# Kernel tuning notes

Hardware: AMD Instinct MI355X
Metric: run time of the kernel (lower is better)

Reference implementation:

```python
import jax, jax.numpy as jnp
from jax import lax
import numpy as np

B, T, D, H, OUT = 128, 1024, 256, 256, 2


def _rnn_layer(inp, W_xh, W_hh, b):
    # inp: [B, T, Din]; returns [B, T, H]
    h0 = jnp.zeros((inp.shape[0], W_hh.shape[0]), inp.dtype)

    def step(h, x_t):
        h_new = jnp.tanh(x_t @ W_xh.T + h @ W_hh.T + b)
        return h_new, h_new

    _, ys = lax.scan(step, h0, jnp.swapaxes(inp, 0, 1))  # ys: [T, B, H]
    return jnp.swapaxes(ys, 0, 1)


def setup_inputs() -> dict:
    key = jax.random.key(0)
    ks = jax.random.split(key, 8)
    s_in = 1.0 / np.sqrt(H)  # torch nn.RNN init scale
    x = jax.random.normal(ks[0], (B, T, D), dtype=jnp.float32)
    W_xh0 = jax.random.uniform(ks[1], (H, D), jnp.float32, -s_in, s_in)
    W_hh0 = jax.random.uniform(ks[2], (H, H), jnp.float32, -s_in, s_in)
    b0 = jax.random.uniform(ks[3], (H,), jnp.float32, -s_in, s_in)
    W_xh1 = jax.random.uniform(ks[4], (H, H), jnp.float32, -s_in, s_in)
    W_hh1 = jax.random.uniform(ks[5], (H, H), jnp.float32, -s_in, s_in)
    b1 = jax.random.uniform(ks[6], (H,), jnp.float32, -s_in, s_in)
    fc_w = jax.random.uniform(ks[7], (OUT, H), jnp.float32, -s_in, s_in)
    fc_b = jnp.zeros((OUT,), jnp.float32)
    return {"x": x, "W_xh0": W_xh0, "W_hh0": W_hh0, "b0": b0,
            "W_xh1": W_xh1, "W_hh1": W_hh1, "b1": b1,
            "fc_w": fc_w, "fc_b": fc_b}


def reference(x, W_xh0, W_hh0, b0, W_xh1, W_hh1, b1, fc_w, fc_b):
    h1 = _rnn_layer(x, W_xh0, W_hh0, b0)   # [B, T, H]
    h2 = _rnn_layer(h1, W_xh1, W_hh1, b1)  # [B, T, H]
    # linear head on last timestep
    return h2[:, -1, :] @ fc_w.T + fc_b    # [B, OUT]
```

## Files before the change

### kernel.cpp

```cpp
#include <hip/hip_runtime.h>

#define Bsz 128
#define Tn  1024
#define Dn  256
#define Hn  256

typedef _Float16 f16;
typedef _Float16 f16x4 __attribute__((ext_vector_type(4)));
typedef _Float16 f16x8 __attribute__((ext_vector_type(8)));
typedef float f32x4 __attribute__((ext_vector_type(4)));

__device__ __forceinline__ float tanh_fast(float x) {
    float e = __builtin_amdgcn_exp2f(x * 2.88539008177793f);
    return 1.0f - 2.0f * __builtin_amdgcn_rcpf(e + 1.0f);
}

__device__ __forceinline__ void wg_barrier() {
    asm volatile("s_waitcnt lgkmcnt(0)\n\ts_barrier" ::: "memory");
}


__global__ __launch_bounds__(256, 2) void k_xproj(
    const float* __restrict__ x, const float* __restrict__ W,
    const float* __restrict__ bias, float* __restrict__ preT)
{
    __shared__ __align__(16) f16 xt[128][264];
    const int tid = threadIdx.x;
    const int t = blockIdx.x;

    for (int i = tid; i < 128 * 64; i += 256) {
        int row = i >> 6, c4 = i & 63;
        float4 v = *(const float4*)(x + ((size_t)row * Tn + t) * Dn + c4 * 4);
        f16x4 tv = { (f16)v.x, (f16)v.y, (f16)v.z, (f16)v.w };
        *(f16x4*)(&xt[row][c4 * 4]) = tv;
    }

    const int lane = tid & 63, l15 = lane & 15, quad = lane >> 4;
    const int w = tid >> 6;

    f16x8 wf[4][8];
    #pragma unroll
    for (int jn = 0; jn < 4; jn++) {
        int j = w * 64 + jn * 16 + l15;
        #pragma unroll
        for (int kk = 0; kk < 8; kk++)
            #pragma unroll
            for (int e = 0; e < 8; e++)
                wf[jn][kk][e] = (f16)W[(size_t)j * Dn + kk * 32 + quad * 8 + e];
    }
    float4 bi[4];
    #pragma unroll
    for (int jn = 0; jn < 4; jn++)
        bi[jn] = *(const float4*)(bias + w * 64 + jn * 16 + quad * 4);

    __syncthreads();

    #pragma unroll 1
    for (int bblk = 0; bblk < 8; bblk++) {
        f32x4 acc[4];
        #pragma unroll
        for (int jn = 0; jn < 4; jn++)
            acc[jn] = (f32x4){bi[jn].x, bi[jn].y, bi[jn].z, bi[jn].w};
        #pragma unroll
        for (int kk = 0; kk < 8; kk++) {
            f16x8 xb = *(const f16x8*)(&xt[bblk * 16 + l15][kk * 32 + quad * 8]);
            #pragma unroll
            for (int jn = 0; jn < 4; jn++)
                acc[jn] = __builtin_amdgcn_mfma_f32_16x16x32_f16(wf[jn][kk], xb, acc[jn], 0, 0, 0);
        }
        #pragma unroll
        for (int jn = 0; jn < 4; jn++) {
            int j0 = w * 64 + jn * 16 + quad * 4;
            *(f32x4*)(preT + ((size_t)t * Bsz + bblk * 16 + l15) * Hn + j0) = acc[jn];
        }
    }
}

__global__ __launch_bounds__(512, 1) void k_fused(
    const float* __restrict__ Whh0, const float* __restrict__ Wxh1,
    const float* __restrict__ Whh1, const float* __restrict__ b1v,
    const float* __restrict__ fcw,  const float* __restrict__ fcb,
    const float* __restrict__ preT, float* __restrict__ out)
{
    __shared__ __align__(16) f16 h1f[2][4096];
    __shared__ __align__(16) f16 h2f[2][4096];

    const int tid  = threadIdx.x;
    const int lane = tid & 63, l15 = lane & 15, quad = lane >> 4;
    const int w    = tid >> 6;
    const int colbase = w * 32;
    const int bg   = blockIdx.x * 16;

    for (int i = tid; i < 4096; i += 512) {
        h1f[0][i] = (f16)0.0f; h1f[1][i] = (f16)0.0f;
        h2f[0][i] = (f16)0.0f; h2f[1][i] = (f16)0.0f;
    }

    f16x8 wh0[2][8], wx[2][8], wh1[2][8];
    #pragma unroll
    for (int jn = 0; jn < 2; jn++) {
        int j = colbase + jn * 16 + l15;
        #pragma unroll
        for (int kk = 0; kk < 8; kk++)
            #pragma unroll
            for (int e = 0; e < 8; e++) {
                int o = (int)((size_t)j * Hn + kk * 32 + quad * 8 + e);
                wh0[jn][kk][e] = (f16)Whh0[o];
                wx [jn][kk][e] = (f16)Wxh1[o];
                wh1[jn][kk][e] = (f16)Whh1[o];
            }
    }
    float4 bi[2];
    #pragma unroll
    for (int jn = 0; jn < 2; jn++)
        bi[jn] = *(const float4*)(b1v + colbase + jn * 16 + quad * 4);

    int wroff[2];
    #pragma unroll
    for (int jn = 0; jn < 2; jn++) {
        int n0 = colbase + jn * 16 + quad * 4;
        wroff[jn] = (n0 >> 5) * 512 + ((n0 >> 3) & 3) * 128 + l15 * 8 + (n0 & 7);
    }

    const float* pp = preT + ((size_t)(bg + l15)) * Hn + colbase + quad * 4;

    f32x4 pnv[2];
    pnv[0] = *(const f32x4*)(pp);
    pnv[1] = *(const f32x4*)(pp + 16);
    __syncthreads();

#define FSTEP_FULL(PR, I, TF) { \
    f32x4 accA[2]; \
    accA[0] = pnv[0]; accA[1] = pnv[1]; \
    pnv[0] = *(const f32x4*)(pp + (size_t)(TF) * (Bsz * Hn)); \
    pnv[1] = *(const f32x4*)(pp + (size_t)(TF) * (Bsz * Hn) + 16); \
    f16x8 hb1[8]; \
    _Pragma("unroll") for (int kk = 0; kk < 8; kk++) { \
        hb1[kk] = *(const f16x8*)(&h1f[(PR)^1][kk * 512 + lane * 8]); \
        accA[0] = __builtin_amdgcn_mfma_f32_16x16x32_f16(wh0[0][kk], hb1[kk], accA[0], 0, 0, 0); \
        accA[1] = __builtin_amdgcn_mfma_f32_16x16x32_f16(wh0[1][kk], hb1[kk], accA[1], 0, 0, 0); \
    } \
     \
    _Pragma("unroll") for (int jn = 0; jn < 2; jn++) { \
        f16x4 t1v = { (f16)tanh_fast(accA[jn][0]), (f16)tanh_fast(accA[jn][1]), \
                      (f16)tanh_fast(accA[jn][2]), (f16)tanh_fast(accA[jn][3]) }; \
        *(f16x4*)(&h1f[(PR)][wroff[jn]]) = t1v; \
    } \
    f32x4 accB[2]; \
    _Pragma("unroll") for (int jn = 0; jn < 2; jn++) \
        accB[jn] = (f32x4){bi[jn].x, bi[jn].y, bi[jn].z, bi[jn].w}; \
    _Pragma("unroll") for (int kk = 0; kk < 8; kk++) { \
        f16x8 hb2 = *(const f16x8*)(&h2f[(PR)][kk * 512 + lane * 8]); \
        accB[0] = __builtin_amdgcn_mfma_f32_16x16x32_f16(wx [0][kk], hb1[kk], accB[0], 0, 0, 0); \
        accB[1] = __builtin_amdgcn_mfma_f32_16x16x32_f16(wx [1][kk], hb1[kk], accB[1], 0, 0, 0); \
        accB[0] = __builtin_amdgcn_mfma_f32_16x16x32_f16(wh1[0][kk], hb2, accB[0], 0, 0, 0); \
        accB[1] = __builtin_amdgcn_mfma_f32_16x16x32_f16(wh1[1][kk], hb2, accB[1], 0, 0, 0); \
    } \
    _Pragma("unroll") for (int jn = 0; jn < 2; jn++) { \
        f16x4 t2v = { (f16)tanh_fast(accB[jn][0]), (f16)tanh_fast(accB[jn][1]), \
                      (f16)tanh_fast(accB[jn][2]), (f16)tanh_fast(accB[jn][3]) }; \
        *(f16x4*)(&h2f[(PR)^1][wroff[jn]]) = t2v; \
    } \
    wg_barrier(); \
}

    {
        f32x4 accA[2];
        accA[0] = pnv[0]; accA[1] = pnv[1];
        pnv[0] = *(const f32x4*)(pp + (size_t)1 * (Bsz * Hn));
        pnv[1] = *(const f32x4*)(pp + (size_t)1 * (Bsz * Hn) + 16);
        #pragma unroll
        for (int kk = 0; kk < 8; kk++) {
            f16x8 hb1 = *(const f16x8*)(&h1f[1][kk * 512 + lane * 8]);
            accA[0] = __builtin_amdgcn_mfma_f32_16x16x32_f16(wh0[0][kk], hb1, accA[0], 0, 0, 0);
            accA[1] = __builtin_amdgcn_mfma_f32_16x16x32_f16(wh0[1][kk], hb1, accA[1], 0, 0, 0);
        }
        #pragma unroll
        for (int jn = 0; jn < 2; jn++) {
            f16x4 t1v = { (f16)tanh_fast(accA[jn][0]), (f16)tanh_fast(accA[jn][1]),
                          (f16)tanh_fast(accA[jn][2]), (f16)tanh_fast(accA[jn][3]) };
            *(f16x4*)(&h1f[0][wroff[jn]]) = t1v;
        }
        wg_barrier();
    }

    #pragma unroll 1
    for (int tp = 0; tp < 511; ++tp) {
        const int t1 = 2 * tp + 1;
        FSTEP_FULL(1, t1, (t1 + 1))
        FSTEP_FULL(0, (t1 + 1), (t1 + 2))
    }
    FSTEP_FULL(1, 1023, 1023)
#undef FSTEP_FULL

    {
        f32x4 accB[2];
        #pragma unroll
        for (int jn = 0; jn < 2; jn++)
            accB[jn] = (f32x4){bi[jn].x, bi[jn].y, bi[jn].z, bi[jn].w};
        #pragma unroll
        for (int kk = 0; kk < 8; kk++) {
            f16x8 hb1 = *(const f16x8*)(&h1f[1][kk * 512 + lane * 8]);
            f16x8 hb2 = *(const f16x8*)(&h2f[0][kk * 512 + lane * 8]);
            accB[0] = __builtin_amdgcn_mfma_f32_16x16x32_f16(wx [0][kk], hb1, accB[0], 0, 0, 0);
            accB[1] = __builtin_amdgcn_mfma_f32_16x16x32_f16(wx [1][kk], hb1, accB[1], 0, 0, 0);
            accB[0] = __builtin_amdgcn_mfma_f32_16x16x32_f16(wh1[0][kk], hb2, accB[0], 0, 0, 0);
            accB[1] = __builtin_amdgcn_mfma_f32_16x16x32_f16(wh1[1][kk], hb2, accB[1], 0, 0, 0);
        }
        #pragma unroll
        for (int jn = 0; jn < 2; jn++) {
            f16x4 t2v = { (f16)tanh_fast(accB[jn][0]), (f16)tanh_fast(accB[jn][1]),
                          (f16)tanh_fast(accB[jn][2]), (f16)tanh_fast(accB[jn][3]) };
            *(f16x4*)(&h2f[1][wroff[jn]]) = t2v;
        }
        wg_barrier();
    }

    if (tid < 256) {
        const int bl = tid >> 4, o = (tid >> 3) & 1, kc = tid & 7;
        float s = 0.f;
        #pragma unroll
        for (int kq = 0; kq < 32; kq++) {
            int k = kc * 32 + kq;
            f16 hv = h2f[1][(k >> 5) * 512 + ((k >> 3) & 3) * 128 + bl * 8 + (k & 7)];
            s += (float)hv * fcw[o * Hn + k];
        }
        s += __shfl_down(s, 4);
        s += __shfl_down(s, 2);
        s += __shfl_down(s, 1);
        if (kc == 0)
            out[(bg + bl) * 2 + o] = s + fcb[o];
    }
}

extern "C" void kernel_launch(void* const* d_in, const int* in_sizes, int n_in,
                              void* d_out, int out_size, void* d_ws, size_t ws_size,
                              hipStream_t stream) {
    const float* x    = (const float*)d_in[0];
    const float* Wxh0 = (const float*)d_in[1];
    const float* Whh0 = (const float*)d_in[2];
    const float* b0   = (const float*)d_in[3];
    const float* Wxh1 = (const float*)d_in[4];
    const float* Whh1 = (const float*)d_in[5];
    const float* b1   = (const float*)d_in[6];
    const float* fcw  = (const float*)d_in[7];
    const float* fcb  = (const float*)d_in[8];
    float* out = (float*)d_out;

    float* preT = (float*)d_ws;

    k_xproj<<<dim3(Tn),       dim3(256), 0, stream>>>(x, Wxh0, b0, preT);
    k_fused<<<dim3(Bsz / 16), dim3(512), 0, stream>>>(Whh0, Wxh1, Whh1, b1,
                                                      fcw, fcb, preT, out);
}
```

Baseline: 1.372 ms.

## Split RNN layers into producer/consumer workgroups pipelined via global memory flags

Layer 0 and layer 1 now run on separate workgroups: 8 producer blocks compute layer-0 hidden states and publish each timestep to a global buffer with a release flag, while 8 consumer blocks spin on the flag and compute layer 1, prefetching the next h1 step from global memory. The goal is to take layer-0 work off layer 1's serial critical path, so each step's dependent chain is shorter and the two layers overlap. In exchange, every step pays global-memory stores and loads plus flag polling latency. The scheme also depends on both producer and consumer blocks being resident at the same time, and the flag is reset to zero at the end so later calls start clean.

```diff
diff --git a/kernel.cpp b/kernel.cpp
--- a/kernel.cpp
+++ b/kernel.cpp
@@ -9,6 +9,11 @@
 typedef _Float16 f16x4 __attribute__((ext_vector_type(4)));
 typedef _Float16 f16x8 __attribute__((ext_vector_type(8)));
 typedef float f32x4 __attribute__((ext_vector_type(4)));
+
+#define MF(A, B, C) __builtin_amdgcn_mfma_f32_16x16x32_f16((A), (B), (C), 0, 0, 0)
+
+__device__ unsigned long long g_h1[8ull * 1024 * 1024];
+__device__ int g_flag[8 * 64];
 
 __device__ __forceinline__ float tanh_fast(float x) {
     float e = __builtin_amdgcn_exp2f(x * 2.88539008177793f);
@@ -66,7 +71,7 @@
             f16x8 xb = *(const f16x8*)(&xt[bblk * 16 + l15][kk * 32 + quad * 8]);
             #pragma unroll
             for (int jn = 0; jn < 4; jn++)
-                acc[jn] = __builtin_amdgcn_mfma_f32_16x16x32_f16(wf[jn][kk], xb, acc[jn], 0, 0, 0);
+                acc[jn] = MF(wf[jn][kk], xb, acc[jn]);
         }
         #pragma unroll
         for (int jn = 0; jn < 4; jn++) {
@@ -82,38 +87,16 @@
     const float* __restrict__ fcw,  const float* __restrict__ fcb,
     const float* __restrict__ preT, float* __restrict__ out)
 {
-    __shared__ __align__(16) f16 h1f[2][4096];
-    __shared__ __align__(16) f16 h2f[2][4096];
+    __shared__ __align__(16) f16 hbuf[2][4096];
 
     const int tid  = threadIdx.x;
     const int lane = tid & 63, l15 = lane & 15, quad = lane >> 4;
     const int w    = tid >> 6;
     const int colbase = w * 32;
-    const int bg   = blockIdx.x * 16;
-
-    for (int i = tid; i < 4096; i += 512) {
-        h1f[0][i] = (f16)0.0f; h1f[1][i] = (f16)0.0f;
-        h2f[0][i] = (f16)0.0f; h2f[1][i] = (f16)0.0f;
-    }
-
-    f16x8 wh0[2][8], wx[2][8], wh1[2][8];
-    #pragma unroll
-    for (int jn = 0; jn < 2; jn++) {
-        int j = colbase + jn * 16 + l15;
-        #pragma unroll
-        for (int kk = 0; kk < 8; kk++)
-            #pragma unroll
-            for (int e = 0; e < 8; e++) {
-                int o = (int)((size_t)j * Hn + kk * 32 + quad * 8 + e);
-                wh0[jn][kk][e] = (f16)Whh0[o];
-                wx [jn][kk][e] = (f16)Wxh1[o];
-                wh1[jn][kk][e] = (f16)Whh1[o];
-            }
-    }
-    float4 bi[2];
-    #pragma unroll
-    for (int jn = 0; jn < 2; jn++)
-        bi[jn] = *(const float4*)(b1v + colbase + jn * 16 + quad * 4);
+    const int gidx = blockIdx.x & 7;
+    const int bg   = gidx * 16;
+
+    for (int i = tid; i < 8192; i += 512) ((f16*)hbuf)[i] = (f16)0.0f;
 
     int wroff[2];
     #pragma unroll
@@ -122,114 +105,177 @@
         wroff[jn] = (n0 >> 5) * 512 + ((n0 >> 3) & 3) * 128 + l15 * 8 + (n0 & 7);
     }
 
-    const float* pp = preT + ((size_t)(bg + l15)) * Hn + colbase + quad * 4;
-
-    f32x4 pnv[2];
-    pnv[0] = *(const f32x4*)(pp);
-    pnv[1] = *(const f32x4*)(pp + 16);
-    __syncthreads();
-
-#define FSTEP_FULL(PR, I, TF) { \
+    unsigned long long* hg = g_h1 + (size_t)gidx * (1024 * 1024);
+    int* flagp = &g_flag[gidx * 64];
+
+    if (blockIdx.x < 8) {
+        f16x8 wh0[2][8];
+        #pragma unroll
+        for (int jn = 0; jn < 2; jn++) {
+            int j = colbase + jn * 16 + l15;
+            #pragma unroll
+            for (int kk = 0; kk < 8; kk++)
+                #pragma unroll
+                for (int e = 0; e < 8; e++)
+                    wh0[jn][kk][e] = (f16)Whh0[(size_t)j * Hn + kk * 32 + quad * 8 + e];
+        }
+        const float* pp = preT + ((size_t)(bg + l15)) * Hn + colbase + quad * 4;
+        f32x4 pnv0 = *(const f32x4*)(pp);
+        f32x4 pnv1 = *(const f32x4*)(pp + 16);
+        __syncthreads();
+
+#define PSTEP(P, I, TF) { \
     f32x4 accA[2]; \
-    accA[0] = pnv[0]; accA[1] = pnv[1]; \
-    pnv[0] = *(const f32x4*)(pp + (size_t)(TF) * (Bsz * Hn)); \
-    pnv[1] = *(const f32x4*)(pp + (size_t)(TF) * (Bsz * Hn) + 16); \
-    f16x8 hb1[8]; \
+    accA[0] = pnv0; accA[1] = pnv1; \
+    pnv0 = *(const f32x4*)(pp + (size_t)(TF) * (Bsz * Hn)); \
+    pnv1 = *(const f32x4*)(pp + (size_t)(TF) * (Bsz * Hn) + 16); \
     _Pragma("unroll") for (int kk = 0; kk < 8; kk++) { \
-        hb1[kk] = *(const f16x8*)(&h1f[(PR)^1][kk * 512 + lane * 8]); \
-        accA[0] = __builtin_amdgcn_mfma_f32_16x16x32_f16(wh0[0][kk], hb1[kk], accA[0], 0, 0, 0); \
-        accA[1] = __builtin_amdgcn_mfma_f32_16x16x32_f16(wh0[1][kk], hb1[kk], accA[1], 0, 0, 0); \
-    } \
-     \
+        f16x8 hb = *(const f16x8*)(&hbuf[(P)^1][kk * 512 + lane * 8]); \
+        accA[0] = MF(wh0[0][kk], hb, accA[0]); \
+        accA[1] = MF(wh0[1][kk], hb, accA[1]); \
+    } \
     _Pragma("unroll") for (int jn = 0; jn < 2; jn++) { \
-        f16x4 t1v = { (f16)tanh_fast(accA[jn][0]), (f16)tanh_fast(accA[jn][1]), \
-                      (f16)tanh_fast(accA[jn][2]), (f16)tanh_fast(accA[jn][3]) }; \
-        *(f16x4*)(&h1f[(PR)][wroff[jn]]) = t1v; \
-    } \
+        union { f16x4 v; unsigned long long u; } t1; \
+        t1.v = (f16x4){ (f16)tanh_fast(accA[jn][0]), (f16)tanh_fast(accA[jn][1]), \
+                        (f16)tanh_fast(accA[jn][2]), (f16)tanh_fast(accA[jn][3]) }; \
+        *(f16x4*)(&hbuf[(P)][wroff[jn]]) = t1.v; \
+        __hip_atomic_store(hg + (size_t)(I) * 1024 + (wroff[jn] >> 2), t1.u, \
+                           __ATOMIC_RELAXED, __HIP_MEMORY_SCOPE_AGENT); \
+    } \
+    asm volatile("s_waitcnt vmcnt(0) lgkmcnt(0)\n\ts_barrier" ::: "memory"); \
+    if (tid == 0) \
+        __hip_atomic_store(flagp, (I) + 1, __ATOMIC_RELEASE, __HIP_MEMORY_SCOPE_AGENT); \
+}
+
+        #pragma unroll 1
+        for (int tp = 0; tp < 511; ++tp) {
+            const int t0 = 2 * tp;
+            PSTEP(0, t0, (t0 + 1))
+            PSTEP(1, (t0 + 1), (t0 + 2))
+        }
+        PSTEP(0, 1022, 1023)
+        PSTEP(1, 1023, 1023)
+#undef PSTEP
+    } else {
+        f16x8 wx[2][8], wh1[2][8];
+        #pragma unroll
+        for (int jn = 0; jn < 2; jn++) {
+            int j = colbase + jn * 16 + l15;
+            #pragma unroll
+            for (int kk = 0; kk < 8; kk++)
+                #pragma unroll
+                for (int e = 0; e < 8; e++) {
+                    int o = (int)((size_t)j * Hn + kk * 32 + quad * 8 + e);
+                    wx [jn][kk][e] = (f16)Wxh1[o];
+                    wh1[jn][kk][e] = (f16)Whh1[o];
+                }
+        }
+        float4 bi[2];
+        #pragma unroll
+        for (int jn = 0; jn < 2; jn++)
+            bi[jn] = *(const float4*)(b1v + colbase + jn * 16 + quad * 4);
+        __syncthreads();
+
+        int fval = __hip_atomic_load(flagp, __ATOMIC_RELAXED, __HIP_MEMORY_SCOPE_AGENT);
+        while (fval < 1) {
+            __builtin_amdgcn_s_sleep(2);
+            fval = __hip_atomic_load(flagp, __ATOMIC_RELAXED, __HIP_MEMORY_SCOPE_AGENT);
+        }
+        __builtin_amdgcn_fence(__ATOMIC_ACQUIRE, "agent");
+        f16x8 bufA[8], bufB[8];
+        {
+            unsigned long long* hp = hg + lane * 2;
+            #pragma unroll
+            for (int kk = 0; kk < 8; kk++) {
+                union { unsigned long long u[2]; f16x8 v; } tb;
+                tb.u[0] = __hip_atomic_load(hp + kk * 128,     __ATOMIC_RELAXED, __HIP_MEMORY_SCOPE_AGENT);
+                tb.u[1] = __hip_atomic_load(hp + kk * 128 + 1, __ATOMIC_RELAXED, __HIP_MEMORY_SCOPE_AGENT);
+                bufA[kk] = tb.v;
+            }
+        }
+        fval = __hip_atomic_load(flagp, __ATOMIC_RELAXED, __HIP_MEMORY_SCOPE_AGENT);
+
+#define CSTEP(P, I, CURB, NXTB) { \
+    int fchk = fval; \
+    fval = __hip_atomic_load(flagp, __ATOMIC_RELAXED, __HIP_MEMORY_SCOPE_AGENT); \
+    if (fchk < (I) + 2) { \
+        do { __builtin_amdgcn_s_sleep(2); \
+             fchk = __hip_atomic_load(flagp, __ATOMIC_RELAXED, __HIP_MEMORY_SCOPE_AGENT); \
+        } while (fchk < (I) + 2); \
+        fval = fchk; \
+    } \
+    __builtin_amdgcn_fence(__ATOMIC_ACQUIRE, "agent"); \
+    { unsigned long long* hp = hg + (size_t)((I) + 1) * 1024 + lane * 2; \
+      _Pragma("unroll") for (int kk = 0; kk < 8; kk++) { \
+        union { unsigned long long u[2]; f16x8 v; } tb; \
+        tb.u[0] = __hip_atomic_load(hp + kk * 128,     __ATOMIC_RELAXED, __HIP_MEMORY_SCOPE_AGENT); \
+        tb.u[1] = __hip_atomic_load(hp + kk * 128 + 1, __ATOMIC_RELAXED, __HIP_MEMORY_SCOPE_AGENT); \
+        NXTB[kk] = tb.v; } } \
     f32x4 accB[2]; \
-    _Pragma("unroll") for (int jn = 0; jn < 2; jn++) \
-        accB[jn] = (f32x4){bi[jn].x, bi[jn].y, bi[jn].z, bi[jn].w}; \
+    accB[0] = (f32x4){bi[0].x, bi[0].y, bi[0].z, bi[0].w}; \
+    accB[1] = (f32x4){bi[1].x, bi[1].y, bi[1].z, bi[1].w}; \
     _Pragma("unroll") for (int kk = 0; kk < 8; kk++) { \
-        f16x8 hb2 = *(const f16x8*)(&h2f[(PR)][kk * 512 + lane * 8]); \
-        accB[0] = __builtin_amdgcn_mfma_f32_16x16x32_f16(wx [0][kk], hb1[kk], accB[0], 0, 0, 0); \
-        accB[1] = __builtin_amdgcn_mfma_f32_16x16x32_f16(wx [1][kk], hb1[kk], accB[1], 0, 0, 0); \
-        accB[0] = __builtin_amdgcn_mfma_f32_16x16x32_f16(wh1[0][kk], hb2, accB[0], 0, 0, 0); \
-        accB[1] = __builtin_amdgcn_mfma_f32_16x16x32_f16(wh1[1][kk], hb2, accB[1], 0, 0, 0); \
+        f16x8 hb2 = *(const f16x8*)(&hbuf[(P)][kk * 512 + lane * 8]); \
+        accB[0] = MF(wx [0][kk], CURB[kk], accB[0]); \
+        accB[1] = MF(wx [1][kk], CURB[kk], accB[1]); \
+        accB[0] = MF(wh1[0][kk], hb2, accB[0]); \
+        accB[1] = MF(wh1[1][kk], hb2, accB[1]); \
     } \
     _Pragma("unroll") for (int jn = 0; jn < 2; jn++) { \
         f16x4 t2v = { (f16)tanh_fast(accB[jn][0]), (f16)tanh_fast(accB[jn][1]), \
                       (f16)tanh_fast(accB[jn][2]), (f16)tanh_fast(accB[jn][3]) }; \
-        *(f16x4*)(&h2f[(PR)^1][wroff[jn]]) = t2v; \
+        *(f16x4*)(&hbuf[(P)^1][wroff[jn]]) = t2v; \
     } \
     wg_barrier(); \
 }
-
-    {
-        f32x4 accA[2];
-        accA[0] = pnv[0]; accA[1] = pnv[1];
-        pnv[0] = *(const f32x4*)(pp + (size_t)1 * (Bsz * Hn));
-        pnv[1] = *(const f32x4*)(pp + (size_t)1 * (Bsz * Hn) + 16);
-        #pragma unroll
-        for (int kk = 0; kk < 8; kk++) {
-            f16x8 hb1 = *(const f16x8*)(&h1f[1][kk * 512 + lane * 8]);
-            accA[0] = __builtin_amdgcn_mfma_f32_16x16x32_f16(wh0[0][kk], hb1, accA[0], 0, 0, 0);
-            accA[1] = __builtin_amdgcn_mfma_f32_16x16x32_f16(wh0[1][kk], hb1, accA[1], 0, 0, 0);
-        }
-        #pragma unroll
-        for (int jn = 0; jn < 2; jn++) {
-            f16x4 t1v = { (f16)tanh_fast(accA[jn][0]), (f16)tanh_fast(accA[jn][1]),
-                          (f16)tanh_fast(accA[jn][2]), (f16)tanh_fast(accA[jn][3]) };
-            *(f16x4*)(&h1f[0][wroff[jn]]) = t1v;
-        }
-        wg_barrier();
-    }
-
-    #pragma unroll 1
-    for (int tp = 0; tp < 511; ++tp) {
-        const int t1 = 2 * tp + 1;
-        FSTEP_FULL(1, t1, (t1 + 1))
-        FSTEP_FULL(0, (t1 + 1), (t1 + 2))
-    }
-    FSTEP_FULL(1, 1023, 1023)
-#undef FSTEP_FULL
-
-    {
-        f32x4 accB[2];
-        #pragma unroll
-        for (int jn = 0; jn < 2; jn++)
-            accB[jn] = (f32x4){bi[jn].x, bi[jn].y, bi[jn].z, bi[jn].w};
-        #pragma unroll
-        for (int kk = 0; kk < 8; kk++) {
-            f16x8 hb1 = *(const f16x8*)(&h1f[1][kk * 512 + lane * 8]);
-            f16x8 hb2 = *(const f16x8*)(&h2f[0][kk * 512 + lane * 8]);
-            accB[0] = __builtin_amdgcn_mfma_f32_16x16x32_f16(wx [0][kk], hb1, accB[0], 0, 0, 0);
-            accB[1] = __builtin_amdgcn_mfma_f32_16x16x32_f16(wx [1][kk], hb1, accB[1], 0, 0, 0);
-            accB[0] = __builtin_amdgcn_mfma_f32_16x16x32_f16(wh1[0][kk], hb2, accB[0], 0, 0, 0);
-            accB[1] = __builtin_amdgcn_mfma_f32_16x16x32_f16(wh1[1][kk], hb2, accB[1], 0, 0, 0);
-        }
-        #pragma unroll
-        for (int jn = 0; jn < 2; jn++) {
-            f16x4 t2v = { (f16)tanh_fast(accB[jn][0]), (f16)tanh_fast(accB[jn][1]),
-                          (f16)tanh_fast(accB[jn][2]), (f16)tanh_fast(accB[jn][3]) };
-            *(f16x4*)(&h2f[1][wroff[jn]]) = t2v;
-        }
-        wg_barrier();
-    }
-
-    if (tid < 256) {
-        const int bl = tid >> 4, o = (tid >> 3) & 1, kc = tid & 7;
-        float s = 0.f;
-        #pragma unroll
-        for (int kq = 0; kq < 32; kq++) {
-            int k = kc * 32 + kq;
-            f16 hv = h2f[1][(k >> 5) * 512 + ((k >> 3) & 3) * 128 + bl * 8 + (k & 7)];
-            s += (float)hv * fcw[o * Hn + k];
-        }
-        s += __shfl_down(s, 4);
-        s += __shfl_down(s, 2);
-        s += __shfl_down(s, 1);
-        if (kc == 0)
-            out[(bg + bl) * 2 + o] = s + fcb[o];
+#define CSTEP_LAST(P, CURB) { \
+    f32x4 accB[2]; \
+    accB[0] = (f32x4){bi[0].x, bi[0].y, bi[0].z, bi[0].w}; \
+    accB[1] = (f32x4){bi[1].x, bi[1].y, bi[1].z, bi[1].w}; \
+    _Pragma("unroll") for (int kk = 0; kk < 8; kk++) { \
+        f16x8 hb2 = *(const f16x8*)(&hbuf[(P)][kk * 512 + lane * 8]); \
+        accB[0] = MF(wx [0][kk], CURB[kk], accB[0]); \
+        accB[1] = MF(wx [1][kk], CURB[kk], accB[1]); \
+        accB[0] = MF(wh1[0][kk], hb2, accB[0]); \
+        accB[1] = MF(wh1[1][kk], hb2, accB[1]); \
+    } \
+    _Pragma("unroll") for (int jn = 0; jn < 2; jn++) { \
+        f16x4 t2v = { (f16)tanh_fast(accB[jn][0]), (f16)tanh_fast(accB[jn][1]), \
+                      (f16)tanh_fast(accB[jn][2]), (f16)tanh_fast(accB[jn][3]) }; \
+        *(f16x4*)(&hbuf[(P)^1][wroff[jn]]) = t2v; \
+    } \
+    wg_barrier(); \
+}
+
+        #pragma unroll 1
+        for (int tp = 0; tp < 511; ++tp) {
+            const int t0 = 2 * tp;
+            CSTEP(0, t0, bufA, bufB)
+            CSTEP(1, (t0 + 1), bufB, bufA)
+        }
+        CSTEP(0, 1022, bufA, bufB)
+        CSTEP_LAST(1, bufB)
+#undef CSTEP
+#undef CSTEP_LAST
+
+        if (tid < 256) {
+            const int bl = tid >> 4, o = (tid >> 3) & 1, kc = tid & 7;
+            float s = 0.f;
+            #pragma unroll
+            for (int kq = 0; kq < 32; kq++) {
+                int k = kc * 32 + kq;
+                f16 hv = hbuf[0][(k >> 5) * 512 + ((k >> 3) & 3) * 128 + bl * 8 + (k & 7)];
+                s += (float)hv * fcw[o * Hn + k];
+            }
+            s += __shfl_down(s, 4);
+            s += __shfl_down(s, 2);
+            s += __shfl_down(s, 1);
+            if (kc == 0)
+                out[(bg + bl) * 2 + o] = s + fcb[o];
+        }
+
+        if (tid == 0)
+            __hip_atomic_store(flagp, 0, __ATOMIC_RELEASE, __HIP_MEMORY_SCOPE_AGENT);
     }
 }
 
@@ -249,7 +295,7 @@
 
     float* preT = (float*)d_ws;
 
-    k_xproj<<<dim3(Tn),       dim3(256), 0, stream>>>(x, Wxh0, b0, preT);
-    k_fused<<<dim3(Bsz / 16), dim3(512), 0, stream>>>(Whh0, Wxh1, Whh1, b1,
-                                                      fcw, fcb, preT, out);
-}
+    k_xproj<<<dim3(Tn), dim3(256), 0, stream>>>(x, Wxh0, b0, preT);
+    k_fused<<<dim3(16), dim3(512), 0, stream>>>(Whh0, Wxh1, Whh1, b1,
+                                                fcw, fcb, preT, out);
+}
```

Measured after the change: 2.443 ms. 1.78x slower.

## Fuse input projection and recurrence into one kernel with per-timestep flags

Applied to the files above, without the earlier changes.

Merges the two launches into a single kernel of 256 blocks. Blocks 0-7 run the two-layer recurrence, while the other 248 blocks compute the layer-0 input projection for timesteps in strided order. Each projection block publishes a per-timestep flag once its preT writes complete, and the recurrence blocks spin on those flags before prefetching the next step's projection. This overlaps the projection phase with the serial recurrence and removes one launch, at the cost of global flags, spin-waits, a completion counter that resets the flags, and a reliance on all blocks being co-resident. Weight loads are also changed to vectorized float4 reads.

```diff
diff --git a/kernel.cpp b/kernel.cpp
--- a/kernel.cpp
+++ b/kernel.cpp
@@ -4,11 +4,20 @@
 #define Tn  1024
 #define Dn  256
 #define Hn  256
+#define NXP 248
 
 typedef _Float16 f16;
 typedef _Float16 f16x4 __attribute__((ext_vector_type(4)));
 typedef _Float16 f16x8 __attribute__((ext_vector_type(8)));
 typedef float f32x4 __attribute__((ext_vector_type(4)));
+typedef unsigned long long u64;
+
+#define MF(A, B, C) __builtin_amdgcn_mfma_f32_16x16x32_f16((A), (B), (C), 0, 0, 0)
+#define ALOAD(p)     __hip_atomic_load((p),      __ATOMIC_RELAXED, __HIP_MEMORY_SCOPE_AGENT)
+#define ASTORE(p, v) __hip_atomic_store((p), (v), __ATOMIC_RELAXED, __HIP_MEMORY_SCOPE_AGENT)
+
+__device__ int g_pflag[1032];
+__device__ int g_done;
 
 __device__ __forceinline__ float tanh_fast(float x) {
     float e = __builtin_amdgcn_exp2f(x * 2.88539008177793f);
@@ -20,95 +29,108 @@
 }
 
 
-__global__ __launch_bounds__(256, 2) void k_xproj(
-    const float* __restrict__ x, const float* __restrict__ W,
-    const float* __restrict__ bias, float* __restrict__ preT)
+__global__ __launch_bounds__(512, 1) void k_all(
+    const float* __restrict__ x,    const float* __restrict__ Wxh0,
+    const float* __restrict__ b0v,  const float* __restrict__ Whh0,
+    const float* __restrict__ Wxh1, const float* __restrict__ Whh1,
+    const float* __restrict__ b1v,  const float* __restrict__ fcw,
+    const float* __restrict__ fcb,  float* __restrict__ preT,
+    float* __restrict__ out)
 {
-    __shared__ __align__(16) f16 xt[128][264];
-    const int tid = threadIdx.x;
-    const int t = blockIdx.x;
-
-    for (int i = tid; i < 128 * 64; i += 256) {
-        int row = i >> 6, c4 = i & 63;
-        float4 v = *(const float4*)(x + ((size_t)row * Tn + t) * Dn + c4 * 4);
-        f16x4 tv = { (f16)v.x, (f16)v.y, (f16)v.z, (f16)v.w };
-        *(f16x4*)(&xt[row][c4 * 4]) = tv;
-    }
-
-    const int lane = tid & 63, l15 = lane & 15, quad = lane >> 4;
-    const int w = tid >> 6;
-
-    f16x8 wf[4][8];
-    #pragma unroll
-    for (int jn = 0; jn < 4; jn++) {
-        int j = w * 64 + jn * 16 + l15;
-        #pragma unroll
-        for (int kk = 0; kk < 8; kk++)
-            #pragma unroll
-            for (int e = 0; e < 8; e++)
-                wf[jn][kk][e] = (f16)W[(size_t)j * Dn + kk * 32 + quad * 8 + e];
-    }
-    float4 bi[4];
-    #pragma unroll
-    for (int jn = 0; jn < 4; jn++)
-        bi[jn] = *(const float4*)(bias + w * 64 + jn * 16 + quad * 4);
-
-    __syncthreads();
-
-    #pragma unroll 1
-    for (int bblk = 0; bblk < 8; bblk++) {
-        f32x4 acc[4];
-        #pragma unroll
-        for (int jn = 0; jn < 4; jn++)
-            acc[jn] = (f32x4){bi[jn].x, bi[jn].y, bi[jn].z, bi[jn].w};
-        #pragma unroll
-        for (int kk = 0; kk < 8; kk++) {
-            f16x8 xb = *(const f16x8*)(&xt[bblk * 16 + l15][kk * 32 + quad * 8]);
-            #pragma unroll
-            for (int jn = 0; jn < 4; jn++)
-                acc[jn] = __builtin_amdgcn_mfma_f32_16x16x32_f16(wf[jn][kk], xb, acc[jn], 0, 0, 0);
-        }
-        #pragma unroll
-        for (int jn = 0; jn < 4; jn++) {
-            int j0 = w * 64 + jn * 16 + quad * 4;
-            *(f32x4*)(preT + ((size_t)t * Bsz + bblk * 16 + l15) * Hn + j0) = acc[jn];
-        }
-    }
-}
-
-__global__ __launch_bounds__(512, 1) void k_fused(
-    const float* __restrict__ Whh0, const float* __restrict__ Wxh1,
-    const float* __restrict__ Whh1, const float* __restrict__ b1v,
-    const float* __restrict__ fcw,  const float* __restrict__ fcb,
-    const float* __restrict__ preT, float* __restrict__ out)
-{
-    __shared__ __align__(16) f16 h1f[2][4096];
-    __shared__ __align__(16) f16 h2f[2][4096];
+    __shared__ __align__(16) f16 smem[128 * 264];
+    __shared__ int sflag;
 
     const int tid  = threadIdx.x;
     const int lane = tid & 63, l15 = lane & 15, quad = lane >> 4;
     const int w    = tid >> 6;
     const int colbase = w * 32;
-    const int bg   = blockIdx.x * 16;
-
-    for (int i = tid; i < 4096; i += 512) {
-        h1f[0][i] = (f16)0.0f; h1f[1][i] = (f16)0.0f;
-        h2f[0][i] = (f16)0.0f; h2f[1][i] = (f16)0.0f;
-    }
+
+    if (blockIdx.x >= 8) {
+        f16 (*xt)[264] = (f16(*)[264])smem;
+        const int w2 = blockIdx.x - 8;
+
+        f16x8 wf[2][8];
+        #pragma unroll
+        for (int jn = 0; jn < 2; jn++) {
+            int j = colbase + jn * 16 + l15;
+            #pragma unroll
+            for (int kk = 0; kk < 8; kk++) {
+                const float* wp = Wxh0 + (size_t)j * Dn + kk * 32 + quad * 8;
+                float4 a = *(const float4*)(wp);
+                float4 b = *(const float4*)(wp + 4);
+                wf[jn][kk] = (f16x8){ (f16)a.x, (f16)a.y, (f16)a.z, (f16)a.w,
+                                      (f16)b.x, (f16)b.y, (f16)b.z, (f16)b.w };
+            }
+        }
+        float4 bx[2];
+        #pragma unroll
+        for (int jn = 0; jn < 2; jn++)
+            bx[jn] = *(const float4*)(b0v + colbase + jn * 16 + quad * 4);
+
+        #pragma unroll 1
+        for (int t = w2; t < Tn; t += NXP) {
+            for (int i = tid; i < 128 * 64; i += 512) {
+                int row = i >> 6, c4 = i & 63;
+                float4 v = *(const float4*)(x + ((size_t)row * Tn + t) * Dn + c4 * 4);
+                f16x4 tv = { (f16)v.x, (f16)v.y, (f16)v.z, (f16)v.w };
+                *(f16x4*)(&xt[row][c4 * 4]) = tv;
+            }
+            __syncthreads();
+
+            #pragma unroll 1
+            for (int bblk = 0; bblk < 8; bblk++) {
+                f32x4 acc[2];
+                #pragma unroll
+                for (int jn = 0; jn < 2; jn++)
+                    acc[jn] = (f32x4){bx[jn].x, bx[jn].y, bx[jn].z, bx[jn].w};
+                #pragma unroll
+                for (int kk = 0; kk < 8; kk++) {
+                    f16x8 xb = *(const f16x8*)(&xt[bblk * 16 + l15][kk * 32 + quad * 8]);
+                    acc[0] = MF(wf[0][kk], xb, acc[0]);
+                    acc[1] = MF(wf[1][kk], xb, acc[1]);
+                }
+                #pragma unroll
+                for (int jn = 0; jn < 2; jn++) {
+                    int j0 = colbase + jn * 16 + quad * 4;
+                    union { f32x4 v; u64 u[2]; } cv; cv.v = acc[jn];
+                    size_t fi = ((size_t)t * Bsz + bblk * 16 + l15) * Hn + j0;
+                    ASTORE((u64*)preT + (fi >> 1),     cv.u[0]);
+                    ASTORE((u64*)preT + (fi >> 1) + 1, cv.u[1]);
+                }
+            }
+            asm volatile("s_waitcnt vmcnt(0)" ::: "memory");
+            __syncthreads();
+            if (tid == 0) ASTORE(&g_pflag[t], 1);
+        }
+        return;
+    }
+
+    f16* h1f0 = smem;
+    f16* h1f1 = smem + 4096;
+    f16* h2f0 = smem + 8192;
+    f16* h2f1 = smem + 12288;
+    const int bg = blockIdx.x * 16;
+
+    for (int i = tid; i < 16384; i += 512) smem[i] = (f16)0.0f;
 
     f16x8 wh0[2][8], wx[2][8], wh1[2][8];
     #pragma unroll
     for (int jn = 0; jn < 2; jn++) {
         int j = colbase + jn * 16 + l15;
         #pragma unroll
-        for (int kk = 0; kk < 8; kk++)
-            #pragma unroll
-            for (int e = 0; e < 8; e++) {
-                int o = (int)((size_t)j * Hn + kk * 32 + quad * 8 + e);
-                wh0[jn][kk][e] = (f16)Whh0[o];
-                wx [jn][kk][e] = (f16)Wxh1[o];
-                wh1[jn][kk][e] = (f16)Whh1[o];
-            }
+        for (int kk = 0; kk < 8; kk++) {
+            size_t o = (size_t)j * Hn + kk * 32 + quad * 8;
+            float4 a, b;
+            a = *(const float4*)(Whh0 + o); b = *(const float4*)(Whh0 + o + 4);
+            wh0[jn][kk] = (f16x8){ (f16)a.x, (f16)a.y, (f16)a.z, (f16)a.w,
+                                   (f16)b.x, (f16)b.y, (f16)b.z, (f16)b.w };
+            a = *(const float4*)(Wxh1 + o); b = *(const float4*)(Wxh1 + o + 4);
+            wx[jn][kk]  = (f16x8){ (f16)a.x, (f16)a.y, (f16)a.z, (f16)a.w,
+                                   (f16)b.x, (f16)b.y, (f16)b.z, (f16)b.w };
+            a = *(const float4*)(Whh1 + o); b = *(const float4*)(Whh1 + o + 4);
+            wh1[jn][kk] = (f16x8){ (f16)a.x, (f16)a.y, (f16)a.z, (f16)a.w,
+                                   (f16)b.x, (f16)b.y, (f16)b.z, (f16)b.w };
+        }
     }
     float4 bi[2];
     #pragma unroll
@@ -122,96 +144,145 @@
         wroff[jn] = (n0 >> 5) * 512 + ((n0 >> 3) & 3) * 128 + l15 * 8 + (n0 & 7);
     }
 
-    const float* pp = preT + ((size_t)(bg + l15)) * Hn + colbase + quad * 4;
-
-    f32x4 pnv[2];
-    pnv[0] = *(const f32x4*)(pp);
-    pnv[1] = *(const f32x4*)(pp + 16);
+    const u64* ppu = (const u64*)preT +
+                     ((((size_t)(bg + l15)) * Hn + colbase + quad * 4) >> 1);
+
+    int fval = ALOAD(&g_pflag[0]);
+    while (fval < 1) { __builtin_amdgcn_s_sleep(8); fval = ALOAD(&g_pflag[0]); }
+    asm volatile("" ::: "memory");
+    u64 pnu0 = ALOAD(ppu),     pnu1 = ALOAD(ppu + 1);
+    u64 pnu2 = ALOAD(ppu + 8), pnu3 = ALOAD(ppu + 9);
+    fval = ALOAD(&g_pflag[1]);
     __syncthreads();
 
-#define FSTEP_FULL(PR, I, TF) { \
+#define UNPACK_ACCA \
     f32x4 accA[2]; \
-    accA[0] = pnv[0]; accA[1] = pnv[1]; \
-    pnv[0] = *(const f32x4*)(pp + (size_t)(TF) * (Bsz * Hn)); \
-    pnv[1] = *(const f32x4*)(pp + (size_t)(TF) * (Bsz * Hn) + 16); \
+    { union { u64 u[2]; f32x4 v; } c0, c1; \
+      c0.u[0] = pnu0; c0.u[1] = pnu1; c1.u[0] = pnu2; c1.u[1] = pnu3; \
+      accA[0] = c0.v; accA[1] = c1.v; }
+
+#define PREFETCH(I) { \
+    int fnew = ALOAD(&g_pflag[(I) + 2]); \
+    if (fval < 1) { \
+        do { __builtin_amdgcn_s_sleep(2); fval = ALOAD(&g_pflag[(I) + 1]); } \
+        while (fval < 1); \
+    } \
+    asm volatile("" ::: "memory"); \
+    const u64* pq = ppu + (size_t)((I) + 1) * ((Bsz * Hn) >> 1); \
+    pnu0 = ALOAD(pq);     pnu1 = ALOAD(pq + 1); \
+    pnu2 = ALOAD(pq + 8); pnu3 = ALOAD(pq + 9); \
+    fval = fnew; }
+
+#define FSTEP(H1R, H1W, H2R, H2W, I) { \
+    UNPACK_ACCA \
+    PREFETCH(I) \
     f16x8 hb1[8]; \
     _Pragma("unroll") for (int kk = 0; kk < 8; kk++) { \
-        hb1[kk] = *(const f16x8*)(&h1f[(PR)^1][kk * 512 + lane * 8]); \
-        accA[0] = __builtin_amdgcn_mfma_f32_16x16x32_f16(wh0[0][kk], hb1[kk], accA[0], 0, 0, 0); \
-        accA[1] = __builtin_amdgcn_mfma_f32_16x16x32_f16(wh0[1][kk], hb1[kk], accA[1], 0, 0, 0); \
-    } \
-     \
+        hb1[kk] = *(const f16x8*)((H1R) + kk * 512 + lane * 8); \
+        accA[0] = MF(wh0[0][kk], hb1[kk], accA[0]); \
+        accA[1] = MF(wh0[1][kk], hb1[kk], accA[1]); \
+    } \
     _Pragma("unroll") for (int jn = 0; jn < 2; jn++) { \
         f16x4 t1v = { (f16)tanh_fast(accA[jn][0]), (f16)tanh_fast(accA[jn][1]), \
                       (f16)tanh_fast(accA[jn][2]), (f16)tanh_fast(accA[jn][3]) }; \
-        *(f16x4*)(&h1f[(PR)][wroff[jn]]) = t1v; \
+        *(f16x4*)((H1W) + wroff[jn]) = t1v; \
     } \
     f32x4 accB[2]; \
-    _Pragma("unroll") for (int jn = 0; jn < 2; jn++) \
-        accB[jn] = (f32x4){bi[jn].x, bi[jn].y, bi[jn].z, bi[jn].w}; \
+    accB[0] = (f32x4){bi[0].x, bi[0].y, bi[0].z, bi[0].w}; \
+    accB[1] = (f32x4){bi[1].x, bi[1].y, bi[1].z, bi[1].w}; \
     _Pragma("unroll") for (int kk = 0; kk < 8; kk++) { \
-        f16x8 hb2 = *(const f16x8*)(&h2f[(PR)][kk * 512 + lane * 8]); \
-        accB[0] = __builtin_amdgcn_mfma_f32_16x16x32_f16(wx [0][kk], hb1[kk], accB[0], 0, 0, 0); \
-        accB[1] = __builtin_amdgcn_mfma_f32_16x16x32_f16(wx [1][kk], hb1[kk], accB[1], 0, 0, 0); \
-        accB[0] = __builtin_amdgcn_mfma_f32_16x16x32_f16(wh1[0][kk], hb2, accB[0], 0, 0, 0); \
-        accB[1] = __builtin_amdgcn_mfma_f32_16x16x32_f16(wh1[1][kk], hb2, accB[1], 0, 0, 0); \
+        f16x8 hb2 = *(const f16x8*)((H2R) + kk * 512 + lane * 8); \
+        accB[0] = MF(wx [0][kk], hb1[kk], accB[0]); \
+        accB[1] = MF(wx [1][kk], hb1[kk], accB[1]); \
+        accB[0] = MF(wh1[0][kk], hb2, accB[0]); \
+        accB[1] = MF(wh1[1][kk], hb2, accB[1]); \
     } \
     _Pragma("unroll") for (int jn = 0; jn < 2; jn++) { \
         f16x4 t2v = { (f16)tanh_fast(accB[jn][0]), (f16)tanh_fast(accB[jn][1]), \
                       (f16)tanh_fast(accB[jn][2]), (f16)tanh_fast(accB[jn][3]) }; \
-        *(f16x4*)(&h2f[(PR)^1][wroff[jn]]) = t2v; \
+        *(f16x4*)((H2W) + wroff[jn]) = t2v; \
     } \
     wg_barrier(); \
 }
 
+#define FSTEP_LAST(H1R, H1W, H2R, H2W) { \
+    UNPACK_ACCA \
+    f16x8 hb1[8]; \
+    _Pragma("unroll") for (int kk = 0; kk < 8; kk++) { \
+        hb1[kk] = *(const f16x8*)((H1R) + kk * 512 + lane * 8); \
+        accA[0] = MF(wh0[0][kk], hb1[kk], accA[0]); \
+        accA[1] = MF(wh0[1][kk], hb1[kk], accA[1]); \
+    } \
+    _Pragma("unroll") for (int jn = 0; jn < 2; jn++) { \
+        f16x4 t1v = { (f16)tanh_fast(accA[jn][0]), (f16)tanh_fast(accA[jn][1]), \
+                      (f16)tanh_fast(accA[jn][2]), (f16)tanh_fast(accA[jn][3]) }; \
+        *(f16x4*)((H1W) + wroff[jn]) = t1v; \
+    } \
+    f32x4 accB[2]; \
+    accB[0] = (f32x4){bi[0].x, bi[0].y, bi[0].z, bi[0].w}; \
+    accB[1] = (f32x4){bi[1].x, bi[1].y, bi[1].z, bi[1].w}; \
+    _Pragma("unroll") for (int kk = 0; kk < 8; kk++) { \
+        f16x8 hb2 = *(const f16x8*)((H2R) + kk * 512 + lane * 8); \
+        accB[0] = MF(wx [0][kk], hb1[kk], accB[0]); \
+        accB[1] = MF(wx [1][kk], hb1[kk], accB[1]); \
+        accB[0] = MF(wh1[0][kk], hb2, accB[0]); \
+        accB[1] = MF(wh1[1][kk], hb2, accB[1]); \
+    } \
+    _Pragma("unroll") for (int jn = 0; jn < 2; jn++) { \
+        f16x4 t2v = { (f16)tanh_fast(accB[jn][0]), (f16)tanh_fast(accB[jn][1]), \
+                      (f16)tanh_fast(accB[jn][2]), (f16)tanh_fast(accB[jn][3]) }; \
+        *(f16x4*)((H2W) + wroff[jn]) = t2v; \
+    } \
+    wg_barrier(); \
+}
+
     {
-        f32x4 accA[2];
-        accA[0] = pnv[0]; accA[1] = pnv[1];
-        pnv[0] = *(const f32x4*)(pp + (size_t)1 * (Bsz * Hn));
-        pnv[1] = *(const f32x4*)(pp + (size_t)1 * (Bsz * Hn) + 16);
+        UNPACK_ACCA
+        PREFETCH(0)
         #pragma unroll
         for (int kk = 0; kk < 8; kk++) {
-            f16x8 hb1 = *(const f16x8*)(&h1f[1][kk * 512 + lane * 8]);
-            accA[0] = __builtin_amdgcn_mfma_f32_16x16x32_f16(wh0[0][kk], hb1, accA[0], 0, 0, 0);
-            accA[1] = __builtin_amdgcn_mfma_f32_16x16x32_f16(wh0[1][kk], hb1, accA[1], 0, 0, 0);
+            f16x8 hb = *(const f16x8*)(h1f1 + kk * 512 + lane * 8);
+            accA[0] = MF(wh0[0][kk], hb, accA[0]);
+            accA[1] = MF(wh0[1][kk], hb, accA[1]);
         }
         #pragma unroll
         for (int jn = 0; jn < 2; jn++) {
             f16x4 t1v = { (f16)tanh_fast(accA[jn][0]), (f16)tanh_fast(accA[jn][1]),
                           (f16)tanh_fast(accA[jn][2]), (f16)tanh_fast(accA[jn][3]) };
-            *(f16x4*)(&h1f[0][wroff[jn]]) = t1v;
+            *(f16x4*)(h1f0 + wroff[jn]) = t1v;
         }
         wg_barrier();
     }
 
     #pragma unroll 1
     for (int tp = 0; tp < 511; ++tp) {
-        const int t1 = 2 * tp + 1;
-        FSTEP_FULL(1, t1, (t1 + 1))
-        FSTEP_FULL(0, (t1 + 1), (t1 + 2))
-    }
-    FSTEP_FULL(1, 1023, 1023)
-#undef FSTEP_FULL
+        FSTEP(h1f0, h1f1, h2f1, h2f0, (2 * tp + 1))
+        FSTEP(h1f1, h1f0, h2f0, h2f1, (2 * tp + 2))
+    }
+    FSTEP_LAST(h1f0, h1f1, h2f1, h2f0)
+#undef FSTEP
+#undef FSTEP_LAST
+#undef PREFETCH
+#undef UNPACK_ACCA
 
     {
         f32x4 accB[2];
-        #pragma unroll
-        for (int jn = 0; jn < 2; jn++)
-            accB[jn] = (f32x4){bi[jn].x, bi[jn].y, bi[jn].z, bi[jn].w};
+        accB[0] = (f32x4){bi[0].x, bi[0].y, bi[0].z, bi[0].w};
+        accB[1] = (f32x4){bi[1].x, bi[1].y, bi[1].z, bi[1].w};
         #pragma unroll
         for (int kk = 0; kk < 8; kk++) {
-            f16x8 hb1 = *(const f16x8*)(&h1f[1][kk * 512 + lane * 8]);
-            f16x8 hb2 = *(const f16x8*)(&h2f[0][kk * 512 + lane * 8]);
-            accB[0] = __builtin_amdgcn_mfma_f32_16x16x32_f16(wx [0][kk], hb1, accB[0], 0, 0, 0);
-            accB[1] = __builtin_amdgcn_mfma_f32_16x16x32_f16(wx [1][kk], hb1, accB[1], 0, 0, 0);
-            accB[0] = __builtin_amdgcn_mfma_f32_16x16x32_f16(wh1[0][kk], hb2, accB[0], 0, 0, 0);
-            accB[1] = __builtin_amdgcn_mfma_f32_16x16x32_f16(wh1[1][kk], hb2, accB[1], 0, 0, 0);
+            f16x8 hb1 = *(const f16x8*)(h1f1 + kk * 512 + lane * 8);
+            f16x8 hb2 = *(const f16x8*)(h2f0 + kk * 512 + lane * 8);
+            accB[0] = MF(wx [0][kk], hb1, accB[0]);
+            accB[1] = MF(wx [1][kk], hb1, accB[1]);
+            accB[0] = MF(wh1[0][kk], hb2, accB[0]);
+            accB[1] = MF(wh1[1][kk], hb2, accB[1]);
         }
         #pragma unroll
         for (int jn = 0; jn < 2; jn++) {
             f16x4 t2v = { (f16)tanh_fast(accB[jn][0]), (f16)tanh_fast(accB[jn][1]),
                           (f16)tanh_fast(accB[jn][2]), (f16)tanh_fast(accB[jn][3]) };
-            *(f16x4*)(&h2f[1][wroff[jn]]) = t2v;
+            *(f16x4*)(h2f1 + wroff[jn]) = t2v;
         }
         wg_barrier();
     }
@@ -222,7 +293,7 @@
         #pragma unroll
         for (int kq = 0; kq < 32; kq++) {
             int k = kc * 32 + kq;
-            f16 hv = h2f[1][(k >> 5) * 512 + ((k >> 3) & 3) * 128 + bl * 8 + (k & 7)];
+            f16 hv = h2f1[(k >> 5) * 512 + ((k >> 3) & 3) * 128 + bl * 8 + (k & 7)];
             s += (float)hv * fcw[o * Hn + k];
         }
         s += __shfl_down(s, 4);
@@ -230,6 +301,17 @@
         s += __shfl_down(s, 1);
         if (kc == 0)
             out[(bg + bl) * 2 + o] = s + fcb[o];
+    }
+
+    __syncthreads();
+    if (tid == 0) {
+        int old = atomicAdd(&g_done, 1);
+        sflag = (old == 7) ? 1 : 0;
+    }
+    __syncthreads();
+    if (sflag) {
+        for (int i = tid; i < 1032; i += 512) ASTORE(&g_pflag[i], 0);
+        if (tid == 0) ASTORE(&g_done, 0);
     }
 }
 
@@ -249,7 +331,6 @@
 
     float* preT = (float*)d_ws;
 
-    k_xproj<<<dim3(Tn),       dim3(256), 0, stream>>>(x, Wxh0, b0, preT);
-    k_fused<<<dim3(Bsz / 16), dim3(512), 0, stream>>>(Whh0, Wxh1, Whh1, b1,
-                                                      fcw, fcb, preT, out);
-}
+    k_all<<<dim3(256), dim3(512), 0, stream>>>(x, Wxh0, b0, Whh0, Wxh1, Whh1,
+                                               b1, fcw, fcb, preT, out);
+}
```

Measured after the change: 1.478 ms. 7.7% more time.

## Restructure input projection: 512 threads, 4 timesteps per block, direct global loads

Applied to the files above, without the earlier changes.

The layer-0 input projection kernel now runs 256 blocks of 512 threads. Each block handles 4 timesteps, with each wave owning 32 output columns, instead of one timestep per 256-thread block staged through shared memory. The fp16 weight fragments are loaded with vectorized float4 reads, and each weight load is amortized over four timesteps. Inputs are read straight from global memory into MFMA fragments, which removes the LDS staging and the block barrier. In exchange, global reads of x are strided per lane and less coalesced than before, and there are fewer blocks for latency hiding. The recurrent kernel, which dominates runtime, only gets a macro rename.

```diff
diff --git a/kernel.cpp b/kernel.cpp
--- a/kernel.cpp
+++ b/kernel.cpp
@@ -10,6 +10,8 @@
 typedef _Float16 f16x8 __attribute__((ext_vector_type(8)));
 typedef float f32x4 __attribute__((ext_vector_type(4)));
 
+#define MF(A, B, C) __builtin_amdgcn_mfma_f32_16x16x32_f16((A), (B), (C), 0, 0, 0)
+
 __device__ __forceinline__ float tanh_fast(float x) {
     float e = __builtin_amdgcn_exp2f(x * 2.88539008177793f);
     return 1.0f - 2.0f * __builtin_amdgcn_rcpf(e + 1.0f);
@@ -20,58 +22,58 @@
 }
 
 
-__global__ __launch_bounds__(256, 2) void k_xproj(
+__global__ __launch_bounds__(512, 1) void k_xproj(
     const float* __restrict__ x, const float* __restrict__ W,
     const float* __restrict__ bias, float* __restrict__ preT)
 {
-    __shared__ __align__(16) f16 xt[128][264];
-    const int tid = threadIdx.x;
-    const int t = blockIdx.x;
-
-    for (int i = tid; i < 128 * 64; i += 256) {
-        int row = i >> 6, c4 = i & 63;
-        float4 v = *(const float4*)(x + ((size_t)row * Tn + t) * Dn + c4 * 4);
-        f16x4 tv = { (f16)v.x, (f16)v.y, (f16)v.z, (f16)v.w };
-        *(f16x4*)(&xt[row][c4 * 4]) = tv;
-    }
-
+    const int tid  = threadIdx.x;
     const int lane = tid & 63, l15 = lane & 15, quad = lane >> 4;
-    const int w = tid >> 6;
-
-    f16x8 wf[4][8];
-    #pragma unroll
-    for (int jn = 0; jn < 4; jn++) {
-        int j = w * 64 + jn * 16 + l15;
-        #pragma unroll
-        for (int kk = 0; kk < 8; kk++)
+    const int w    = tid >> 6;
+    const int colbase = w * 32;
+
+    f16x8 wf[2][8];
+    #pragma unroll
+    for (int jn = 0; jn < 2; jn++) {
+        int j = colbase + jn * 16 + l15;
+        #pragma unroll
+        for (int kk = 0; kk < 8; kk++) {
+            const float* wp = W + (size_t)j * Dn + kk * 32 + quad * 8;
+            float4 a = *(const float4*)(wp);
+            float4 b = *(const float4*)(wp + 4);
+            wf[jn][kk] = (f16x8){ (f16)a.x, (f16)a.y, (f16)a.z, (f16)a.w,
+                                  (f16)b.x, (f16)b.y, (f16)b.z, (f16)b.w };
+        }
+    }
+    float4 bx[2];
+    #pragma unroll
+    for (int jn = 0; jn < 2; jn++)
+        bx[jn] = *(const float4*)(bias + colbase + jn * 16 + quad * 4);
+
+    #pragma unroll 1
+    for (int tt = 0; tt < 4; tt++) {
+        const int t = blockIdx.x * 4 + tt;
+        #pragma unroll
+        for (int bblk = 0; bblk < 8; bblk++) {
+            const float* xp = x + ((size_t)(bblk * 16 + l15) * Tn + t) * Dn + quad * 8;
+            f16x8 xb[8];
             #pragma unroll
-            for (int e = 0; e < 8; e++)
-                wf[jn][kk][e] = (f16)W[(size_t)j * Dn + kk * 32 + quad * 8 + e];
-    }
-    float4 bi[4];
-    #pragma unroll
-    for (int jn = 0; jn < 4; jn++)
-        bi[jn] = *(const float4*)(bias + w * 64 + jn * 16 + quad * 4);
-
-    __syncthreads();
-
-    #pragma unroll 1
-    for (int bblk = 0; bblk < 8; bblk++) {
-        f32x4 acc[4];
-        #pragma unroll
-        for (int jn = 0; jn < 4; jn++)
-            acc[jn] = (f32x4){bi[jn].x, bi[jn].y, bi[jn].z, bi[jn].w};
-        #pragma unroll
-        for (int kk = 0; kk < 8; kk++) {
-            f16x8 xb = *(const f16x8*)(&xt[bblk * 16 + l15][kk * 32 + quad * 8]);
+            for (int kk = 0; kk < 8; kk++) {
+                float4 a = *(const float4*)(xp + kk * 32);
+                float4 b = *(const float4*)(xp + kk * 32 + 4);
+                xb[kk] = (f16x8){ (f16)a.x, (f16)a.y, (f16)a.z, (f16)a.w,
+                                  (f16)b.x, (f16)b.y, (f16)b.z, (f16)b.w };
+            }
+            f32x4 acc0 = (f32x4){bx[0].x, bx[0].y, bx[0].z, bx[0].w};
+            f32x4 acc1 = (f32x4){bx[1].x, bx[1].y, bx[1].z, bx[1].w};
             #pragma unroll
-            for (int jn = 0; jn < 4; jn++)
-                acc[jn] = __builtin_amdgcn_mfma_f32_16x16x32_f16(wf[jn][kk], xb, acc[jn], 0, 0, 0);
-        }
-        #pragma unroll
-        for (int jn = 0; jn < 4; jn++) {
-            int j0 = w * 64 + jn * 16 + quad * 4;
-            *(f32x4*)(preT + ((size_t)t * Bsz + bblk * 16 + l15) * Hn + j0) = acc[jn];
+            for (int kk = 0; kk < 8; kk++) {
+                acc0 = MF(wf[0][kk], xb[kk], acc0);
+                acc1 = MF(wf[1][kk], xb[kk], acc1);
+            }
+            float* pp = preT + ((size_t)t * Bsz + bblk * 16 + l15) * Hn
+                             + colbase + quad * 4;
+            *(f32x4*)(pp)      = acc0;
+            *(f32x4*)(pp + 16) = acc1;
         }
     }
 }
@@ -137,8 +139,8 @@
     f16x8 hb1[8]; \
     _Pragma("unroll") for (int kk = 0; kk < 8; kk++) { \
         hb1[kk] = *(const f16x8*)(&h1f[(PR)^1][kk * 512 + lane * 8]); \
-        accA[0] = __builtin_amdgcn_mfma_f32_16x16x32_f16(wh0[0][kk], hb1[kk], accA[0], 0, 0, 0); \
-        accA[1] = __builtin_amdgcn_mfma_f32_16x16x32_f16(wh0[1][kk], hb1[kk], accA[1], 0, 0, 0); \
+        accA[0] = MF(wh0[0][kk], hb1[kk], accA[0]); \
+        accA[1] = MF(wh0[1][kk], hb1[kk], accA[1]); \
     } \
      \
     _Pragma("unroll") for (int jn = 0; jn < 2; jn++) { \
@@ -151,10 +153,10 @@
         accB[jn] = (f32x4){bi[jn].x, bi[jn].y, bi[jn].z, bi[jn].w}; \
     _Pragma("unroll") for (int kk = 0; kk < 8; kk++) { \
         f16x8 hb2 = *(const f16x8*)(&h2f[(PR)][kk * 512 + lane * 8]); \
-        accB[0] = __builtin_amdgcn_mfma_f32_16x16x32_f16(wx [0][kk], hb1[kk], accB[0], 0, 0, 0); \
-        accB[1] = __builtin_amdgcn_mfma_f32_16x16x32_f16(wx [1][kk], hb1[kk], accB[1], 0, 0, 0); \
-        accB[0] = __builtin_amdgcn_mfma_f32_16x16x32_f16(wh1[0][kk], hb2, accB[0], 0, 0, 0); \
-        accB[1] = __builtin_amdgcn_mfma_f32_16x16x32_f16(wh1[1][kk], hb2, accB[1], 0, 0, 0); \
+        accB[0] = MF(wx [0][kk], hb1[kk], accB[0]); \
+        accB[1] = MF(wx [1][kk], hb1[kk], accB[1]); \
+        accB[0] = MF(wh1[0][kk], hb2, accB[0]); \
+        accB[1] = MF(wh1[1][kk], hb2, accB[1]); \
     } \
     _Pragma("unroll") for (int jn = 0; jn < 2; jn++) { \
         f16x4 t2v = { (f16)tanh_fast(accB[jn][0]), (f16)tanh_fast(accB[jn][1]), \
@@ -172,8 +174,8 @@
         #pragma unroll
         for (int kk = 0; kk < 8; kk++) {
             f16x8 hb1 = *(const f16x8*)(&h1f[1][kk * 512 + lane * 8]);
-            accA[0] = __builtin_amdgcn_mfma_f32_16x16x32_f16(wh0[0][kk], hb1, accA[0], 0, 0, 0);
-            accA[1] = __builtin_amdgcn_mfma_f32_16x16x32_f16(wh0[1][kk], hb1, accA[1], 0, 0, 0);
+            accA[0] = MF(wh0[0][kk], hb1, accA[0]);
+            accA[1] = MF(wh0[1][kk], hb1, accA[1]);
         }
         #pragma unroll
         for (int jn = 0; jn < 2; jn++) {
@@ -202,10 +204,10 @@
         for (int kk = 0; kk < 8; kk++) {
             f16x8 hb1 = *(const f16x8*)(&h1f[1][kk * 512 + lane * 8]);
             f16x8 hb2 = *(const f16x8*)(&h2f[0][kk * 512 + lane * 8]);
-            accB[0] = __builtin_amdgcn_mfma_f32_16x16x32_f16(wx [0][kk], hb1, accB[0], 0, 0, 0);
-            accB[1] = __builtin_amdgcn_mfma_f32_16x16x32_f16(wx [1][kk], hb1, accB[1], 0, 0, 0);
-            accB[0] = __builtin_amdgcn_mfma_f32_16x16x32_f16(wh1[0][kk], hb2, accB[0], 0, 0, 0);
-            accB[1] = __builtin_amdgcn_mfma_f32_16x16x32_f16(wh1[1][kk], hb2, accB[1], 0, 0, 0);
+            accB[0] = MF(wx [0][kk], hb1, accB[0]);
+            accB[1] = MF(wx [1][kk], hb1, accB[1]);
+            accB[0] = MF(wh1[0][kk], hb2, accB[0]);
+            accB[1] = MF(wh1[1][kk], hb2, accB[1]);
         }
         #pragma unroll
         for (int jn = 0; jn < 2; jn++) {
@@ -249,7 +251,7 @@
 
     float* preT = (float*)d_ws;
 
-    k_xproj<<<dim3(Tn),       dim3(256), 0, stream>>>(x, Wxh0, b0, preT);
+    k_xproj<<<dim3(256), dim3(512), 0, stream>>>(x, Wxh0, b0, preT);
     k_fused<<<dim3(Bsz / 16), dim3(512), 0, stream>>>(Whh0, Wxh1, Whh1, b1,
                                                       fcw, fcb, preT, out);
 }
```

New measurement: 1.455 ms. 6.0% more time.
